# Performance work log

Measured on AMD Instinct MI355X. Metric: run time of the kernel, lower is better.

## Reference

```python
import jax, jax.numpy as jnp
import numpy as np

A = 5          # num anchors
C = 80         # num classes
STRIDE = 16    # network stride
THRESH = 0.6
OBJ_SCALE = 5.0
NOOBJ_SCALE = 1.0
COORD_SCALE = 1.0
CLASS_SCALE = 1.0


def setup_inputs() -> dict:
    key = jax.random.key(0)
    k1, k2, k3, k4 = jax.random.split(key, 4)
    B, H, W, N = 16, 64, 64, 50
    output = jax.random.normal(k1, (B, A * (5 + C), H, W), dtype=jnp.float32)
    cls_id = jax.random.randint(k2, (B, N, 1), 0, C).astype(jnp.float32)
    cxcy = jax.random.uniform(k3, (B, N, 2), dtype=jnp.float32) * (W * STRIDE)
    wh = jax.random.uniform(k4, (B, N, 2), dtype=jnp.float32) * 290.0 + 10.0
    target = jnp.concatenate([cls_id, cxcy, wh], axis=-1)  # (B, N, 5)
    anchors = jnp.array([[18.3, 21.6], [60.0, 66.0], [106.8, 175.5],
                         [252.2, 112.9], [312.7, 293.4]], dtype=jnp.float32)
    return {"output": output, "target": target, "anchors": anchors}


def _iou(g, p):
    # g: (B, N, 4), p: (B, M, 4), boxes in [cx, cy, w, h]
    gx1, gy1 = g[..., 0] - g[..., 2] / 2, g[..., 1] - g[..., 3] / 2
    gx2, gy2 = g[..., 0] + g[..., 2] / 2, g[..., 1] + g[..., 3] / 2
    px1, py1 = p[..., 0] - p[..., 2] / 2, p[..., 1] - p[..., 3] / 2
    px2, py2 = p[..., 0] + p[..., 2] / 2, p[..., 1] + p[..., 3] / 2
    ix1 = jnp.maximum(gx1[:, :, None], px1[:, None, :])
    iy1 = jnp.maximum(gy1[:, :, None], py1[:, None, :])
    ix2 = jnp.minimum(gx2[:, :, None], px2[:, None, :])
    iy2 = jnp.minimum(gy2[:, :, None], py2[:, None, :])
    inter = jnp.clip(ix2 - ix1, 0) * jnp.clip(iy2 - iy1, 0)
    g_area = (gx2 - gx1) * (gy2 - gy1)
    p_area = (px2 - px1) * (py2 - py1)
    union = g_area[:, :, None] + p_area[:, None, :] - inter + 1e-6
    return inter / union  # (B, N, M)


def reference(output, target, anchors):
    B, _, H, W = output.shape
    out = output.reshape(B, A, 5 + C, H, W).transpose(0, 1, 3, 4, 2)  # (B,A,H,W,5+C)
    coord = out[..., :4]
    conf = out[..., 4]
    cls_logits = out[..., 5:]

    gx = jnp.arange(W, dtype=output.dtype)
    gy = jnp.arange(H, dtype=output.dtype)
    px = (jax.nn.sigmoid(coord[..., 0]) + gx[None, None, None, :]) * STRIDE
    py = (jax.nn.sigmoid(coord[..., 1]) + gy[None, None, :, None]) * STRIDE
    pw = jnp.exp(coord[..., 2]) * anchors[:, 0][None, :, None, None]
    ph = jnp.exp(coord[..., 3]) * anchors[:, 1][None, :, None, None]
    pred_boxes = jnp.stack([px, py, pw, ph], axis=-1).reshape(B, -1, 4)  # (B, A*H*W, 4)

    gt_boxes = target[..., 1:]  # (B, N, 4)
    gt_cls = target[..., 0]     # (B, N)

    iou = _iou(gt_boxes, pred_boxes)          # (B, N, M)
    best_iou = iou.max(axis=1)                # (B, M)
    best_idx = iou.argmax(axis=1)             # (B, M)

    mask = (best_iou > THRESH).reshape(B, A, H, W)
    mask_f = mask.astype(output.dtype)
    conf_mask = jnp.where(mask, OBJ_SCALE, NOOBJ_SCALE).astype(output.dtype)

    tcoord = jnp.take_along_axis(gt_boxes, best_idx[..., None], axis=1)  # (B, M, 4)
    tcoord = tcoord.reshape(B, A, H, W, 4) * mask_f[..., None]
    tcls = jnp.take_along_axis(gt_cls, best_idx, axis=1).reshape(B, A, H, W)
    tcls_idx = (tcls * mask_f).astype(jnp.int32)
    tconf = mask_f

    cm = mask_f[..., None]
    coord_loss = COORD_SCALE * jnp.sum((coord * cm - tcoord * cm) ** 2)
    conf_loss = jnp.sum((conf * conf_mask - tconf * conf_mask) ** 2)
    logp = jax.nn.log_softmax(cls_logits, axis=-1)
    nll = -jnp.take_along_axis(logp, tcls_idx[..., None], axis=-1)[..., 0]
    cls_loss = CLASS_SCALE * jnp.sum(jnp.where(mask, nll, 0.0))

    return coord_loss + conf_loss + cls_loss
```

## Files before the change

kernel.cpp:

```cpp
#include <hip/hip_runtime.h>

#define A_   5
#define C_   80
#define BB   16
#define HH   64
#define WW   64
#define NN   50
#define CH   (5 + C_)
#define HW   (HH * WW)
#define STRIDE_F 16.0f

#define NWAVES (BB * A_ * HH)
#define NBLK   (NWAVES / 2)

#define GBOX_OFF   0
#define GAREA_OFF  (BB * NN * 4)
#define PART_OFF   (GAREA_OFF + BB * NN)

__global__ __launch_bounds__(256)
void region_prep(const float* __restrict__ target, float* __restrict__ ws)
{
    int i = threadIdx.x + blockIdx.x * 256;
    if (i < BB * NN) {
        const float* t = target + (size_t)i * 5;
        float cx = t[1], cy = t[2], gw = t[3], gh = t[4];
        float4* gbox = (float4*)(ws + GBOX_OFF);
        gbox[i] = make_float4(cx - 0.5f * gw, cy - 0.5f * gh,
                              cx + 0.5f * gw, cy + 0.5f * gh);
        ws[GAREA_OFF + i] = gw * gh;
    }
}

__global__ __launch_bounds__(128)
void region_loss_main(const float* __restrict__ out4d,
                      const float* __restrict__ target,
                      const float* __restrict__ anchors,
                      const float* __restrict__ ws,
                      float* __restrict__ partial)
{
    const int tid  = threadIdx.x;
    const int lane = tid & 63;
    const int wv   = tid >> 6;
    const int gwid = blockIdx.x * 2 + wv;
    const int h    = gwid & 63;
    const int a    = (gwid >> 6) % A_;
    const int b    = gwid / (A_ * HH);

    const size_t plane = ((size_t)b * A_ + a) * CH * HW;
    const float* base  = out4d + plane + (size_t)h * WW + lane;

    const float x0 = base[0 * HW];
    const float x1 = base[1 * HW];
    const float x2 = base[2 * HW];
    const float x3 = base[3 * HW];
    const float cf = base[4 * HW];

    const float aw = anchors[a * 2 + 0];
    const float ah = anchors[a * 2 + 1];

    const float px = (1.0f / (1.0f + __expf(-x0)) + (float)lane) * STRIDE_F;
    const float py = (1.0f / (1.0f + __expf(-x1)) + (float)h) * STRIDE_F;
    const float pw = __expf(x2) * aw;
    const float ph = __expf(x3) * ah;
    const float px1 = px - 0.5f * pw, py1 = py - 0.5f * ph;
    const float px2 = px + 0.5f * pw, py2 = py + 0.5f * ph;
    const float parea = pw * ph;

    const float4* gb_b = (const float4*)(ws + GBOX_OFF) + b * NN;
    const float*  ga_b = ws + GAREA_OFF + b * NN;

    float bi = 0.0f, bu = 1.0f;
    int   bn = 0;
    #pragma unroll 2
    for (int n = 0; n < NN; ++n) {
        const float4 gb = gb_b[n];
        const float  ga = ga_b[n];
        float ix1 = fmaxf(gb.x, px1);
        float iy1 = fmaxf(gb.y, py1);
        float ix2 = fminf(gb.z, px2);
        float iy2 = fminf(gb.w, py2);
        float iw  = fmaxf(ix2 - ix1, 0.0f);
        float ih  = fmaxf(iy2 - iy1, 0.0f);
        float inter = iw * ih;
        float uni   = ga + parea - inter + 1e-6f;
        if (inter * bu > bi * uni) {
            bi = inter; bu = uni; bn = n;
        }
    }
    const bool mask = bi > 0.6f * bu;

    float local;
    int tcls = 0;
    if (mask) {
        const float* t = target + ((size_t)b * NN + bn) * 5;
        float d0 = x0 - t[1];
        float d1 = x1 - t[2];
        float d2 = x2 - t[3];
        float d3 = x3 - t[4];
        float cd = 5.0f * cf - 5.0f;
        local = d0*d0 + d1*d1 + d2*d2 + d3*d3 + cd*cd;
        tcls = (int)t[0];
    } else {
        local = cf * cf;
    }

    if (__ballot(mask) != 0ull) {
        const float* cb = base + 5 * HW;
        float s0 = 0.f, s1 = 0.f, s2 = 0.f, s3 = 0.f;
        #pragma unroll 4
        for (int c = 0; c < C_; c += 4) {
            s0 += __expf(cb[(c + 0) * HW]);
            s1 += __expf(cb[(c + 1) * HW]);
            s2 += __expf(cb[(c + 2) * HW]);
            s3 += __expf(cb[(c + 3) * HW]);
        }
        if (mask) {
            const float xt = cb[tcls * HW];
            local += __logf((s0 + s1) + (s2 + s3)) - xt;
        }
    }

    for (int off = 32; off > 0; off >>= 1)
        local += __shfl_down(local, off);
    if (lane == 0) partial[gwid] = local;
}

__global__ __launch_bounds__(256)
void region_loss_finalize(const float* __restrict__ partial, float* __restrict__ out)
{
    __shared__ float wsum[4];
    const int tid = threadIdx.x;
    float s = 0.0f;
    for (int i = tid; i < NWAVES; i += 256)
        s += partial[i];
    for (int off = 32; off > 0; off >>= 1)
        s += __shfl_down(s, off);
    if ((tid & 63) == 0) wsum[tid >> 6] = s;
    __syncthreads();
    if (tid == 0) out[0] = wsum[0] + wsum[1] + wsum[2] + wsum[3];
}

extern "C" void kernel_launch(void* const* d_in, const int* in_sizes, int n_in,
                              void* d_out, int out_size, void* d_ws, size_t ws_size,
                              hipStream_t stream) {
    const float* output  = (const float*)d_in[0];
    const float* target  = (const float*)d_in[1];
    const float* anchors = (const float*)d_in[2];
    float* loss = (float*)d_out;
    float* ws   = (float*)d_ws;

    region_prep<<<(BB * NN + 255) / 256, 256, 0, stream>>>(target, ws);
    region_loss_main<<<NBLK, 128, 0, stream>>>(output, target, anchors,
                                               ws, ws + PART_OFF);
    region_loss_finalize<<<1, 256, 0, stream>>>(ws + PART_OFF, loss);
}
```

Baseline: 171.5 us.

## Fuse final reduction into main kernel via atomics and drop finalize launch

Removes the separate finalize kernel: each 256-thread block reduces four wave sums in shared memory and atomically adds into the output, which the prep kernel zeroes. Block size goes from 128 to 256 threads. The class log-softmax loop now runs only on masked lanes instead of the whole wave whenever any lane is masked. This saves a launch and a partial-buffer round trip, at the cost of atomic contention on one address and nondeterministic float summation order.

Result: no change. 169.3 us (-1.3%).

```diff
diff --git a/kernel.cpp b/kernel.cpp
--- a/kernel.cpp
+++ b/kernel.cpp
@@ -10,17 +10,15 @@
 #define HW   (HH * WW)
 #define STRIDE_F 16.0f
 
-#define NWAVES (BB * A_ * HH)
-#define NBLK   (NWAVES / 2)
-
 #define GBOX_OFF   0
 #define GAREA_OFF  (BB * NN * 4)
-#define PART_OFF   (GAREA_OFF + BB * NN)
 
 __global__ __launch_bounds__(256)
-void region_prep(const float* __restrict__ target, float* __restrict__ ws)
+void region_prep(const float* __restrict__ target, float* __restrict__ ws,
+                 float* __restrict__ loss)
 {
-    int i = threadIdx.x + blockIdx.x * 256;
+    const int i = threadIdx.x + blockIdx.x * 256;
+    if (i == 0) loss[0] = 0.0f;
     if (i < BB * NN) {
         const float* t = target + (size_t)i * 5;
         float cx = t[1], cy = t[2], gw = t[3], gh = t[4];
@@ -31,17 +29,18 @@
     }
 }
 
-__global__ __launch_bounds__(128)
+__global__ __launch_bounds__(256)
 void region_loss_main(const float* __restrict__ out4d,
                       const float* __restrict__ target,
                       const float* __restrict__ anchors,
                       const float* __restrict__ ws,
-                      float* __restrict__ partial)
+                      float* __restrict__ loss)
 {
+    __shared__ float wsum[4];
     const int tid  = threadIdx.x;
     const int lane = tid & 63;
     const int wv   = tid >> 6;
-    const int gwid = blockIdx.x * 2 + wv;
+    const int gwid = blockIdx.x * 4 + wv;
     const int h    = gwid & 63;
     const int a    = (gwid >> 6) % A_;
     const int b    = gwid / (A_ * HH);
@@ -90,7 +89,6 @@
     const bool mask = bi > 0.6f * bu;
 
     float local;
-    int tcls = 0;
     if (mask) {
         const float* t = target + ((size_t)b * NN + bn) * 5;
         float d0 = x0 - t[1];
@@ -99,12 +97,8 @@
         float d3 = x3 - t[4];
         float cd = 5.0f * cf - 5.0f;
         local = d0*d0 + d1*d1 + d2*d2 + d3*d3 + cd*cd;
-        tcls = (int)t[0];
-    } else {
-        local = cf * cf;
-    }
 
-    if (__ballot(mask) != 0ull) {
+        const int tcls = (int)t[0];
         const float* cb = base + 5 * HW;
         float s0 = 0.f, s1 = 0.f, s2 = 0.f, s3 = 0.f;
         #pragma unroll 4
@@ -114,30 +108,17 @@
             s2 += __expf(cb[(c + 2) * HW]);
             s3 += __expf(cb[(c + 3) * HW]);
         }
-        if (mask) {
-            const float xt = cb[tcls * HW];
-            local += __logf((s0 + s1) + (s2 + s3)) - xt;
-        }
+        local += __logf((s0 + s1) + (s2 + s3)) - cb[tcls * HW];
+    } else {
+        local = cf * cf;
     }
 
     for (int off = 32; off > 0; off >>= 1)
         local += __shfl_down(local, off);
-    if (lane == 0) partial[gwid] = local;
-}
-
-__global__ __launch_bounds__(256)
-void region_loss_finalize(const float* __restrict__ partial, float* __restrict__ out)
-{
-    __shared__ float wsum[4];
-    const int tid = threadIdx.x;
-    float s = 0.0f;
-    for (int i = tid; i < NWAVES; i += 256)
-        s += partial[i];
-    for (int off = 32; off > 0; off >>= 1)
-        s += __shfl_down(s, off);
-    if ((tid & 63) == 0) wsum[tid >> 6] = s;
+    if (lane == 0) wsum[wv] = local;
     __syncthreads();
-    if (tid == 0) out[0] = wsum[0] + wsum[1] + wsum[2] + wsum[3];
+    if (tid == 0)
+        atomicAdd(loss, wsum[0] + wsum[1] + wsum[2] + wsum[3]);
 }
 
 extern "C" void kernel_launch(void* const* d_in, const int* in_sizes, int n_in,
@@ -149,8 +130,7 @@
     float* loss = (float*)d_out;
     float* ws   = (float*)d_ws;
 
-    region_prep<<<(BB * NN + 255) / 256, 256, 0, stream>>>(target, ws);
-    region_loss_main<<<NBLK, 128, 0, stream>>>(output, target, anchors,
-                                               ws, ws + PART_OFF);
-    region_loss_finalize<<<1, 256, 0, stream>>>(ws + PART_OFF, loss);
+    region_prep<<<(BB * NN + 255) / 256, 256, 0, stream>>>(target, ws, loss);
+    region_loss_main<<<BB * A_ * HH / 4, 256, 0, stream>>>(output, target, anchors,
+                                                           ws, loss);
 }
```
